# Kernel tuning notes

Hardware: AMD Instinct MI355X
Metric: run time of the kernel (lower is better)

## Reference

```python
import jax, jax.numpy as jnp
import numpy as np

B, N, F, F1 = 1024, 75, 512, 256
NEG = -1.0e9
ALPHA = 0.2  # LeakyReLU slope


def setup_inputs() -> dict:
    key = jax.random.key(0)
    k1, k2, k3, k4 = jax.random.split(key, 4)
    X = jax.random.normal(k1, (B, N, F), dtype=jnp.float32)
    A = jax.random.randint(k2, (N, N), 0, 2, dtype=jnp.int32)  # binary adjacency
    W = jax.random.normal(k3, (F, F1), dtype=jnp.float32) * (1.0 / np.sqrt(F))
    a = jax.random.normal(k4, (2, F1, 1), dtype=jnp.float32) * (1.0 / np.sqrt(F1))
    return {"X": X, "A": A, "W": W, "a": a}


def reference(X, A, W, a):
    # Linear projection: [B, N, F1]
    h = jnp.einsum('bnf,fo->bno', X, W)
    # Additive attention logits
    att_self = jnp.einsum('bno,od->bnd', h, a[0])        # [B, N, 1]
    att_neigh = jnp.einsum('bno,od->bnd', h, a[1])       # [B, N, 1]
    e = att_self + jnp.swapaxes(att_neigh, 1, 2)         # [B, N, N]
    e = jax.nn.leaky_relu(e, ALPHA)
    # Adjacency mask: disallowed edges get large negative bias
    adj = A.astype(h.dtype)                               # [N, N]
    e = e + NEG * (1.0 - adj)[None, :, :]
    # Normalize over neighbors, aggregate
    alpha = jax.nn.softmax(e, axis=-1)                    # [B, N, N]
    out = jnp.einsum('bij,bjo->bio', alpha, h)            # [B, N, F1]
    return jnp.concatenate([out, h], axis=-1)             # [B, N, 2*F1]
```

## Files before the change

kernel.cpp:

```cpp
#include <hip/hip_runtime.h>
#include <hip/hip_bf16.h>
#include <math.h>

typedef __bf16 bf16_t;
typedef __bf16 bf16x4_t __attribute__((ext_vector_type(4)));
typedef __bf16 bf16x8 __attribute__((ext_vector_type(8)));
typedef float f32x4 __attribute__((ext_vector_type(4)));
typedef unsigned long long u64;

#define NB 1024
#define NN 75
#define KF 512
#define F1 256
#define HSTR 100
#define ASTR 100

__global__ __launch_bounds__(256) void wt_kernel(const float* __restrict__ W,
                                                 bf16_t* __restrict__ Wt) {
    __shared__ float tile[64][65];
    const int kb = blockIdx.x * 64;
    const int nb = blockIdx.y * 64;
    const int tc = threadIdx.x & 63;
    const int tr = threadIdx.x >> 6;
#pragma unroll
    for (int r = tr; r < 64; r += 4)
        tile[r][tc] = W[(size_t)(kb + r) * F1 + nb + tc];
    __syncthreads();
#pragma unroll
    for (int r = tr; r < 64; r += 4)
        Wt[(size_t)(nb + r) * KF + kb + tc] = (bf16_t)tile[tc][r];
}

__global__ __launch_bounds__(256) void gemm_kernel(const float* __restrict__ X,
                                                   const bf16_t* __restrict__ Wt,
                                                   float* __restrict__ out) {
    __shared__ __align__(16) char smem[40960];
    bf16_t* Xb = (bf16_t*)smem;
    bf16_t* Wb = (bf16_t*)(smem + 8192);

    const int t = threadIdx.x;
    const int w = t >> 6;
    const int l = t & 63;
    const int lc = l & 15;
    const int lr = l >> 4;
    const int m0 = blockIdx.x * 64;

    const int xrow  = ((t >> 6) << 4) + (t & 15);
    const int kpart = ((t >> 4) & 3) * 8;
    const float* xsrc = X + (size_t)(m0 + xrow) * KF + kpart;
    const bf16_t* wsrc0 = Wt + (size_t)(((t >> 6) + 0) * 16 + (t & 15)) * KF + kpart;
    const bf16_t* wsrc1 = Wt + (size_t)(((t >> 6) + 4) * 16 + (t & 15)) * KF + kpart;
    const bf16_t* wsrc2 = Wt + (size_t)(((t >> 6) + 8) * 16 + (t & 15)) * KF + kpart;
    const bf16_t* wsrc3 = Wt + (size_t)(((t >> 6) + 12) * 16 + (t & 15)) * KF + kpart;

    f32x4 acc[4][4];
#pragma unroll
    for (int i = 0; i < 4; ++i)
#pragma unroll
        for (int j = 0; j < 4; ++j) acc[i][j] = (f32x4){0.f, 0.f, 0.f, 0.f};

    {
        const float4 xa = *(const float4*)xsrc;
        const float4 xb = *(const float4*)(xsrc + 4);
        bf16x8 v;
        v[0]=(bf16_t)xa.x; v[1]=(bf16_t)xa.y; v[2]=(bf16_t)xa.z; v[3]=(bf16_t)xa.w;
        v[4]=(bf16_t)xb.x; v[5]=(bf16_t)xb.y; v[6]=(bf16_t)xb.z; v[7]=(bf16_t)xb.w;
        *(bf16x8*)&Xb[t * 8] = v;
        *(uint4*)&Wb[t * 8 + 0 * 2048] = *(const uint4*)wsrc0;
        *(uint4*)&Wb[t * 8 + 1 * 2048] = *(const uint4*)wsrc1;
        *(uint4*)&Wb[t * 8 + 2 * 2048] = *(const uint4*)wsrc2;
        *(uint4*)&Wb[t * 8 + 3 * 2048] = *(const uint4*)wsrc3;
    }
    __syncthreads();

    for (int ks = 0; ks < 16; ++ks) {
        const int cur = ks & 1;
        float4 xa, xb;
        uint4 wv0, wv1, wv2, wv3;
        if (ks < 15) {
            const int k1 = (ks + 1) * 32;
            xa = *(const float4*)(xsrc + k1);
            xb = *(const float4*)(xsrc + k1 + 4);
            wv0 = *(const uint4*)(wsrc0 + k1);
            wv1 = *(const uint4*)(wsrc1 + k1);
            wv2 = *(const uint4*)(wsrc2 + k1);
            wv3 = *(const uint4*)(wsrc3 + k1);
        }
        const bf16_t* Xc = Xb + cur * 2048;
        const bf16_t* Wc = Wb + cur * 8192;
        bf16x8 af[4], bv[4];
#pragma unroll
        for (int mt = 0; mt < 4; ++mt)
            af[mt] = *(const bf16x8*)&Xc[(mt * 64 + l) * 8];
#pragma unroll
        for (int ntl = 0; ntl < 4; ++ntl)
            bv[ntl] = *(const bf16x8*)&Wc[((w * 4 + ntl) * 64 + l) * 8];
#pragma unroll
        for (int mt = 0; mt < 4; ++mt)
#pragma unroll
            for (int ntl = 0; ntl < 4; ++ntl)
                acc[mt][ntl] = __builtin_amdgcn_mfma_f32_16x16x32_bf16(af[mt], bv[ntl], acc[mt][ntl], 0, 0, 0);
        if (ks < 15) {
            const int nxt = cur ^ 1;
            bf16_t* Xn = Xb + nxt * 2048;
            bf16_t* Wn = Wb + nxt * 8192;
            bf16x8 v;
            v[0]=(bf16_t)xa.x; v[1]=(bf16_t)xa.y; v[2]=(bf16_t)xa.z; v[3]=(bf16_t)xa.w;
            v[4]=(bf16_t)xb.x; v[5]=(bf16_t)xb.y; v[6]=(bf16_t)xb.z; v[7]=(bf16_t)xb.w;
            *(bf16x8*)&Xn[t * 8] = v;
            *(uint4*)&Wn[t * 8 + 0 * 2048] = wv0;
            *(uint4*)&Wn[t * 8 + 1 * 2048] = wv1;
            *(uint4*)&Wn[t * 8 + 2 * 2048] = wv2;
            *(uint4*)&Wn[t * 8 + 3 * 2048] = wv3;
        }
        __syncthreads();
    }

#pragma unroll
    for (int mt = 0; mt < 4; ++mt) {
#pragma unroll
        for (int ntl = 0; ntl < 4; ++ntl) {
            const int col = w * 64 + ntl * 16 + lc;
#pragma unroll
            for (int j = 0; j < 4; ++j) {
                const int row = m0 + mt * 16 + lr * 4 + j;
                out[(size_t)row * 512 + 256 + col] = acc[mt][ntl][j];
            }
        }
    }
}

__global__ __launch_bounds__(256) void pv_kernel(const int* __restrict__ Adj,
                                                 const float* __restrict__ avec,
                                                 float* __restrict__ out) {
    __shared__ __align__(16) bf16_t hT[256 * HSTR];
    __shared__ __align__(16) bf16_t alp[80 * ASTR];
    __shared__ float a0s[F1], a1s[F1];
    __shared__ float attp0[4][80], attp1[4][80];
    __shared__ float att0s[80], att1s[80], rsums[80];
    __shared__ u64 adjb[160];

    const int b = blockIdx.x;
    const int t = threadIdx.x;
    const int w = t >> 6;
    const int l = t & 63;
    const int lc = l & 15;
    const int lr = l >> 4;
    float* outb = out + (size_t)b * NN * 512;

    a0s[t] = avec[t];
    a1s[t] = avec[F1 + t];
    for (int i = w; i < NN; i += 4) {
        const int v0 = Adj[i * NN + l];
        const int v1 = (l < NN - 64) ? Adj[i * NN + 64 + l] : 0;
        const u64 b0 = __ballot(v0 != 0);
        const u64 b1 = __ballot(v1 != 0);
        if (l == 0) { adjb[i * 2] = b0; adjb[i * 2 + 1] = b1; }
    }
    {
        int* z = (int*)&hT[t * HSTR + 80];
#pragma unroll
        for (int k = 0; k < 8; ++k) z[k] = 0;
    }
    __syncthreads();

    const int c0 = w * 64 + lc * 4;
    const float4 a04 = *(const float4*)&a0s[c0];
    const float4 a14 = *(const float4*)&a1s[c0];
#pragma unroll
    for (int jp = 0; jp < 5; ++jp) {
        const int j0 = jp * 16 + lr * 4;
        float hr[4][4];
#pragma unroll
        for (int r = 0; r < 4; ++r) {
            if (j0 + r < NN) {
                const float4 v = *(const float4*)(outb + (size_t)(j0 + r) * 512 + 256 + c0);
                hr[r][0] = v.x; hr[r][1] = v.y; hr[r][2] = v.z; hr[r][3] = v.w;
            } else {
                hr[r][0] = hr[r][1] = hr[r][2] = hr[r][3] = 0.f;
            }
        }
        float p0[4], p1[4];
#pragma unroll
        for (int r = 0; r < 4; ++r) {
            p0[r] = hr[r][0] * a04.x + hr[r][1] * a04.y + hr[r][2] * a04.z + hr[r][3] * a04.w;
            p1[r] = hr[r][0] * a14.x + hr[r][1] * a14.y + hr[r][2] * a14.z + hr[r][3] * a14.w;
        }
#pragma unroll
        for (int off = 1; off < 16; off <<= 1) {
#pragma unroll
            for (int r = 0; r < 4; ++r) {
                p0[r] += __shfl_xor(p0[r], off);
                p1[r] += __shfl_xor(p1[r], off);
            }
        }
        if (lc == 0) {
#pragma unroll
            for (int r = 0; r < 4; ++r) {
                attp0[w][j0 + r] = p0[r];
                attp1[w][j0 + r] = p1[r];
            }
        }
#pragma unroll
        for (int cc = 0; cc < 4; ++cc) {
            bf16x4_t v;
            v[0] = (bf16_t)hr[0][cc]; v[1] = (bf16_t)hr[1][cc];
            v[2] = (bf16_t)hr[2][cc]; v[3] = (bf16_t)hr[3][cc];
            *(bf16x4_t*)&hT[(c0 + cc) * HSTR + j0] = v;
        }
    }
    __syncthreads();

    if (t < 80)
        att0s[t] = attp0[0][t] + attp0[1][t] + attp0[2][t] + attp0[3][t];
    else if (t < 160)
        att1s[t - 80] = attp1[0][t - 80] + attp1[1][t - 80] + attp1[2][t - 80] + attp1[3][t - 80];
    else if (t < 240) {
        const int r = t - 160;
        if (r < NN) {
            for (int c = NN; c < 96; ++c) alp[r * ASTR + c] = (bf16_t)0.f;
        } else {
            for (int c = 0; c < 96; ++c) alp[r * ASTR + c] = (bf16_t)0.f;
        }
    }
    __syncthreads();

    {
        const int gid = t >> 2;
        const int k4 = t & 3;
#pragma unroll
        for (int r = 0; r < 2; ++r) {
            const int i = r * 64 + gid;
            if (i < NN) {
                const float a0i = att0s[i];
                const u64 w0 = adjb[i * 2];
                const u64 w1 = adjb[i * 2 + 1];
                float e[19];
                float m = -3.0e38f;
#pragma unroll
                for (int jj = 0; jj < 19; ++jj) {
                    const int j = jj * 4 + k4;
                    float ev = -3.0e38f;
                    if (j < NN) {
                        float x = a0i + att1s[j];
                        x = x > 0.f ? x : 0.2f * x;
                        const u64 wj = (j < 64) ? w0 : w1;
                        const int bit = (int)((wj >> (j & 63)) & 1);
                        ev = bit ? x : x - 1.0e9f;
                    }
                    e[jj] = ev;
                    m = fmaxf(m, ev);
                }
                m = fmaxf(m, __shfl_xor(m, 1));
                m = fmaxf(m, __shfl_xor(m, 2));
                float s = 0.f;
#pragma unroll
                for (int jj = 0; jj < 19; ++jj) {
                    const int j = jj * 4 + k4;
                    if (j < NN) {
                        const float ex = __expf(e[jj] - m);
                        s += ex;
                        alp[i * ASTR + j] = (bf16_t)ex;
                    }
                }
                s += __shfl_xor(s, 1);
                s += __shfl_xor(s, 2);
                if (k4 == 0) rsums[i] = 1.f / s;
            }
        }
    }
    __syncthreads();

    f32x4 acc2[5][4];
#pragma unroll
    for (int i = 0; i < 5; ++i)
#pragma unroll
        for (int j = 0; j < 4; ++j) acc2[i][j] = (f32x4){0.f, 0.f, 0.f, 0.f};

#pragma unroll
    for (int ks = 0; ks < 3; ++ks) {
        bf16x8 bv[4];
#pragma unroll
        for (int ntl = 0; ntl < 4; ++ntl) {
            const bf16_t* q = &hT[(w * 64 + ntl * 16 + lc) * HSTR + ks * 32 + lr * 8];
            ((uint2*)&bv[ntl])[0] = *(const uint2*)q;
            ((uint2*)&bv[ntl])[1] = *(const uint2*)(q + 4);
        }
#pragma unroll
        for (int mt = 0; mt < 5; ++mt) {
            const bf16_t* ap = &alp[(mt * 16 + lc) * ASTR + ks * 32 + lr * 8];
            bf16x8 av;
            ((uint2*)&av)[0] = *(const uint2*)ap;
            ((uint2*)&av)[1] = *(const uint2*)(ap + 4);
#pragma unroll
            for (int ntl = 0; ntl < 4; ++ntl)
                acc2[mt][ntl] = __builtin_amdgcn_mfma_f32_16x16x32_bf16(av, bv[ntl], acc2[mt][ntl], 0, 0, 0);
        }
    }

#pragma unroll
    for (int mt = 0; mt < 5; ++mt) {
#pragma unroll
        for (int j = 0; j < 4; ++j) {
            const int row = mt * 16 + lr * 4 + j;
            if (row < NN) {
                const float rsv = rsums[row];
#pragma unroll
                for (int ntl = 0; ntl < 4; ++ntl) {
                    const int ch = w * 64 + ntl * 16 + lc;
                    outb[(size_t)row * 512 + ch] = acc2[mt][ntl][j] * rsv;
                }
            }
        }
    }
}

extern "C" void kernel_launch(void* const* d_in, const int* in_sizes, int n_in,
                              void* d_out, int out_size, void* d_ws, size_t ws_size,
                              hipStream_t stream) {
    const float* X = (const float*)d_in[0];
    const int*   A = (const int*)d_in[1];
    const float* W = (const float*)d_in[2];
    const float* a = (const float*)d_in[3];
    float* out = (float*)d_out;
    bf16_t* Wt = (bf16_t*)d_ws;

    wt_kernel<<<dim3(KF / 64, F1 / 64), 256, 0, stream>>>(W, Wt);
    gemm_kernel<<<(NB * NN) / 64, 256, 0, stream>>>(X, Wt, out);
    pv_kernel<<<NB, 256, 0, stream>>>(A, a, out);
}
```

Before: 144.1 us.

## Load W fragments directly to registers and deepen X prefetch in GEMM

The GEMM kernel stops staging W in shared memory. Each wave now loads its B-operand fragments straight from global memory into registers, using ping-pong register buffers one k-step ahead. X global loads are also issued two steps ahead and the k-loop is fully unrolled in pairs. This cuts shared memory from 40KB to 8KB and removes the LDS writes and reads for W, which may raise occupancy. In exchange each wave re-reads W from global/L2 memory, and register pressure goes up.

```diff
diff --git a/kernel.cpp b/kernel.cpp
--- a/kernel.cpp
+++ b/kernel.cpp
@@ -34,9 +34,7 @@
 __global__ __launch_bounds__(256) void gemm_kernel(const float* __restrict__ X,
                                                    const bf16_t* __restrict__ Wt,
                                                    float* __restrict__ out) {
-    __shared__ __align__(16) char smem[40960];
-    bf16_t* Xb = (bf16_t*)smem;
-    bf16_t* Wb = (bf16_t*)(smem + 8192);
+    __shared__ __align__(16) bf16_t Xb[2 * 2048];
 
     const int t = threadIdx.x;
     const int w = t >> 6;
@@ -48,10 +46,11 @@
     const int xrow  = ((t >> 6) << 4) + (t & 15);
     const int kpart = ((t >> 4) & 3) * 8;
     const float* xsrc = X + (size_t)(m0 + xrow) * KF + kpart;
-    const bf16_t* wsrc0 = Wt + (size_t)(((t >> 6) + 0) * 16 + (t & 15)) * KF + kpart;
-    const bf16_t* wsrc1 = Wt + (size_t)(((t >> 6) + 4) * 16 + (t & 15)) * KF + kpart;
-    const bf16_t* wsrc2 = Wt + (size_t)(((t >> 6) + 8) * 16 + (t & 15)) * KF + kpart;
-    const bf16_t* wsrc3 = Wt + (size_t)(((t >> 6) + 12) * 16 + (t & 15)) * KF + kpart;
+
+    const bf16_t* wp0 = Wt + (size_t)(w * 64 + 0 * 16 + lc) * KF + lr * 8;
+    const bf16_t* wp1 = Wt + (size_t)(w * 64 + 1 * 16 + lc) * KF + lr * 8;
+    const bf16_t* wp2 = Wt + (size_t)(w * 64 + 2 * 16 + lc) * KF + lr * 8;
+    const bf16_t* wp3 = Wt + (size_t)(w * 64 + 3 * 16 + lc) * KF + lr * 8;
 
     f32x4 acc[4][4];
 #pragma unroll
@@ -59,62 +58,67 @@
 #pragma unroll
         for (int j = 0; j < 4; ++j) acc[i][j] = (f32x4){0.f, 0.f, 0.f, 0.f};
 
+    float4 xa, xb;
+    bf16x8 wA[4], wB[4];
+
+#define WLOAD(WREG, KS)                                        \
+    WREG[0] = *(const bf16x8*)(wp0 + (KS) * 32);               \
+    WREG[1] = *(const bf16x8*)(wp1 + (KS) * 32);               \
+    WREG[2] = *(const bf16x8*)(wp2 + (KS) * 32);               \
+    WREG[3] = *(const bf16x8*)(wp3 + (KS) * 32);
+
+#define GSTEP(KS, WREG)                                                        \
+    {                                                                          \
+        const bf16_t* Xc = Xb + ((KS) & 1) * 2048;                             \
+        bf16x8 af[4];                                                          \
+        _Pragma("unroll")                                                      \
+        for (int mt = 0; mt < 4; ++mt)                                         \
+            af[mt] = *(const bf16x8*)&Xc[(mt * 64 + l) * 8];                   \
+        _Pragma("unroll")                                                      \
+        for (int mt = 0; mt < 4; ++mt)                                         \
+            _Pragma("unroll")                                                  \
+            for (int ntl = 0; ntl < 4; ++ntl)                                  \
+                acc[mt][ntl] = __builtin_amdgcn_mfma_f32_16x16x32_bf16(        \
+                    af[mt], WREG[ntl], acc[mt][ntl], 0, 0, 0);                 \
+        if ((KS) < 15) {                                                       \
+            bf16x8 v;                                                          \
+            v[0]=(bf16_t)xa.x; v[1]=(bf16_t)xa.y;                              \
+            v[2]=(bf16_t)xa.z; v[3]=(bf16_t)xa.w;                              \
+            v[4]=(bf16_t)xb.x; v[5]=(bf16_t)xb.y;                              \
+            v[6]=(bf16_t)xb.z; v[7]=(bf16_t)xb.w;                              \
+            *(bf16x8*)&Xb[(((KS) + 1) & 1) * 2048 + t * 8] = v;                \
+            if ((KS) < 14) {                                                   \
+                xa = *(const float4*)(xsrc + ((KS) + 2) * 32);                 \
+                xb = *(const float4*)(xsrc + ((KS) + 2) * 32 + 4);             \
+            }                                                                  \
+        }                                                                      \
+        __syncthreads();                                                       \
+    }
+
+    WLOAD(wA, 0);
     {
-        const float4 xa = *(const float4*)xsrc;
-        const float4 xb = *(const float4*)(xsrc + 4);
+        xa = *(const float4*)xsrc;
+        xb = *(const float4*)(xsrc + 4);
         bf16x8 v;
         v[0]=(bf16_t)xa.x; v[1]=(bf16_t)xa.y; v[2]=(bf16_t)xa.z; v[3]=(bf16_t)xa.w;
         v[4]=(bf16_t)xb.x; v[5]=(bf16_t)xb.y; v[6]=(bf16_t)xb.z; v[7]=(bf16_t)xb.w;
         *(bf16x8*)&Xb[t * 8] = v;
-        *(uint4*)&Wb[t * 8 + 0 * 2048] = *(const uint4*)wsrc0;
-        *(uint4*)&Wb[t * 8 + 1 * 2048] = *(const uint4*)wsrc1;
-        *(uint4*)&Wb[t * 8 + 2 * 2048] = *(const uint4*)wsrc2;
-        *(uint4*)&Wb[t * 8 + 3 * 2048] = *(const uint4*)wsrc3;
-    }
-    __syncthreads();
-
-    for (int ks = 0; ks < 16; ++ks) {
-        const int cur = ks & 1;
-        float4 xa, xb;
-        uint4 wv0, wv1, wv2, wv3;
-        if (ks < 15) {
-            const int k1 = (ks + 1) * 32;
-            xa = *(const float4*)(xsrc + k1);
-            xb = *(const float4*)(xsrc + k1 + 4);
-            wv0 = *(const uint4*)(wsrc0 + k1);
-            wv1 = *(const uint4*)(wsrc1 + k1);
-            wv2 = *(const uint4*)(wsrc2 + k1);
-            wv3 = *(const uint4*)(wsrc3 + k1);
-        }
-        const bf16_t* Xc = Xb + cur * 2048;
-        const bf16_t* Wc = Wb + cur * 8192;
-        bf16x8 af[4], bv[4];
-#pragma unroll
-        for (int mt = 0; mt < 4; ++mt)
-            af[mt] = *(const bf16x8*)&Xc[(mt * 64 + l) * 8];
-#pragma unroll
-        for (int ntl = 0; ntl < 4; ++ntl)
-            bv[ntl] = *(const bf16x8*)&Wc[((w * 4 + ntl) * 64 + l) * 8];
-#pragma unroll
-        for (int mt = 0; mt < 4; ++mt)
-#pragma unroll
-            for (int ntl = 0; ntl < 4; ++ntl)
-                acc[mt][ntl] = __builtin_amdgcn_mfma_f32_16x16x32_bf16(af[mt], bv[ntl], acc[mt][ntl], 0, 0, 0);
-        if (ks < 15) {
-            const int nxt = cur ^ 1;
-            bf16_t* Xn = Xb + nxt * 2048;
-            bf16_t* Wn = Wb + nxt * 8192;
-            bf16x8 v;
-            v[0]=(bf16_t)xa.x; v[1]=(bf16_t)xa.y; v[2]=(bf16_t)xa.z; v[3]=(bf16_t)xa.w;
-            v[4]=(bf16_t)xb.x; v[5]=(bf16_t)xb.y; v[6]=(bf16_t)xb.z; v[7]=(bf16_t)xb.w;
-            *(bf16x8*)&Xn[t * 8] = v;
-            *(uint4*)&Wn[t * 8 + 0 * 2048] = wv0;
-            *(uint4*)&Wn[t * 8 + 1 * 2048] = wv1;
-            *(uint4*)&Wn[t * 8 + 2 * 2048] = wv2;
-            *(uint4*)&Wn[t * 8 + 3 * 2048] = wv3;
-        }
-        __syncthreads();
-    }
+        xa = *(const float4*)(xsrc + 32);
+        xb = *(const float4*)(xsrc + 36);
+    }
+    __syncthreads();
+
+#pragma unroll
+    for (int kp = 0; kp < 8; ++kp) {
+        const int ks0 = kp * 2;
+        const int ks1 = kp * 2 + 1;
+        WLOAD(wB, ks1);
+        GSTEP(ks0, wA);
+        if (ks1 < 15) { WLOAD(wA, ks1 + 1); }
+        GSTEP(ks1, wB);
+    }
+#undef GSTEP
+#undef WLOAD
 
 #pragma unroll
     for (int mt = 0; mt < 4; ++mt) {
```

New measurement: 141.0 us. 1.02x faster.
